# Performance work log

Hardware: AMD Instinct MI355X
Metric: run time of the kernel (lower is better)

## Reference

```python
import jax, jax.numpy as jnp
import numpy as np

B, IN, OUT, P = 512, 4096, 4096, 4
BITS = 4
MAX_INT = float(2 ** (BITS - 1) - 1)  # 7.0


def setup_inputs() -> dict:
    key = jax.random.key(0)
    k1, k2, k3, k4 = jax.random.split(key, 4)
    x = jax.random.normal(k1, (B, IN), dtype=jnp.float32)
    # Cached LFSR-generated pseudo-random matrix, values normalized to [-1, 1]
    U = jax.random.uniform(k2, (OUT * IN, P), dtype=jnp.float32, minval=-1.0, maxval=1.0)
    # 4-bit quantized projection: integers in [-7, 7] stored as float
    q = jnp.round(jnp.clip(jax.random.normal(k3, (P,), dtype=jnp.float32) * 3.0, -MAX_INT, MAX_INT))
    b = jax.random.normal(k4, (OUT,), dtype=jnp.float32)
    return {"x": x, "U": U, "q": q, "b": b, "exponent": 0}


def reference(x, U, q, b, exponent):
    # dequantize: t_hat = q / max_int * 2^exponent  (shared-exponent 4-bit dequant)
    scale = jnp.float32(2.0) ** exponent
    t_hat = q / MAX_INT * scale                      # [P]
    # reconstruct full weight: W = U @ t_hat, reshape to (out, in)
    w = (U @ t_hat).reshape(OUT, IN)                 # [OUT, IN]
    # original layer forward (nn.Linear): y = x @ W^T + b
    return x @ w.T + b                               # [B, OUT]
```

## Files before the change

### kernel.cpp

```cpp
#include <hip/hip_runtime.h>

typedef unsigned short ushort_t;
typedef unsigned int uint_t;
typedef __attribute__((ext_vector_type(4))) float f32x4;
typedef __attribute__((ext_vector_type(8))) short bf16x8;

#define B_DIM 512
#define IN_DIM 4096
#define OUT_DIM 4096
#define BN 32
#define BK 32
#define KSPLIT 4

__device__ __forceinline__ ushort_t f2bf(float f) {
    union { float f; uint_t u; } v; v.f = f;
    uint_t r = v.u + 0x7fffu + ((v.u >> 16) & 1u);
    return (ushort_t)(r >> 16);
}

__global__ __launch_bounds__(256) void conv_x(const float4* __restrict__ X4,
                                              ushort_t* __restrict__ Xb) {
    size_t i = (size_t)blockIdx.x * 256 + threadIdx.x;
    float4 a = X4[i];
    ushort_t r[4] = { f2bf(a.x), f2bf(a.y), f2bf(a.z), f2bf(a.w) };
    *(uint2*)(Xb + i * 4) = *(const uint2*)r;
}

__global__ __launch_bounds__(256, 2) void gemm_pipe(
    const ushort_t* __restrict__ A,
    const float4* __restrict__ U4,
    const float* __restrict__ q,
    const int* __restrict__ expo,
    float* __restrict__ part)
{
    const int M = B_DIM, N = OUT_DIM, K = IN_DIM;
    __shared__ ushort_t sW[2 * BN * BK];

    const int tid  = threadIdx.x;
    const int lane = tid & 63;
    const int wave = tid >> 6;
    const int quad = lane >> 4;
    const int r16  = lane & 15;

    const int n0 = blockIdx.x * BN;
    const int kseg = K / KSPLIT;
    const size_t kbase = (size_t)blockIdx.y * kseg;
    const int nsteps = kseg / BK;

    const float scale = exp2f((float)expo[0]) * (1.0f / 7.0f);
    const float t0 = q[0] * scale, t1 = q[1] * scale,
                t2 = q[2] * scale, t3 = q[3] * scale;

    const float4* gU = U4 + (size_t)(n0 + (tid >> 3)) * K + kbase + (tid & 7) * 4;
    ushort_t* lWb = sW + (tid >> 3) * BK + (tid & 7) * 4;

    const ushort_t* pa = A + (size_t)(wave * 128 + r16) * K + kbase + quad * 8;
    const ushort_t* fb = sW + r16 * BK + quad * 8;

    f32x4 acc[8][2] = {};

    float4 uc[4];
#pragma unroll
    for (int c = 0; c < 4; ++c) uc[c] = gU[c];

#pragma unroll 1
    for (int s = 0; s < nsteps; ++s) {
        bf16x8 av[8];
#pragma unroll
        for (int i = 0; i < 8; ++i)
            av[i] = *(const bf16x8*)(pa + (size_t)i * 16 * K + (size_t)s * BK);

        const size_t koff = (size_t)((s + 1 < nsteps) ? (s + 1) : s) * BK;
        float4 un[4];
#pragma unroll
        for (int c = 0; c < 4; ++c) un[c] = gU[koff + c];

        ushort_t wv[4];
#pragma unroll
        for (int c = 0; c < 4; ++c)
            wv[c] = f2bf(uc[c].x * t0 + uc[c].y * t1 + uc[c].z * t2 + uc[c].w * t3);
        *(uint2*)(lWb + (s & 1) * (BN * BK)) = *(const uint2*)wv;

        asm volatile("s_waitcnt lgkmcnt(0)" ::: "memory");
        __builtin_amdgcn_s_barrier();

        const ushort_t* fbs = fb + (s & 1) * (BN * BK);
        bf16x8 bv0 = *(const bf16x8*)(fbs);
        bf16x8 bv1 = *(const bf16x8*)(fbs + 16 * BK);

#pragma unroll
        for (int i = 0; i < 8; ++i) {
            acc[i][0] = __builtin_amdgcn_mfma_f32_16x16x32_bf16(av[i], bv0, acc[i][0], 0, 0, 0);
            acc[i][1] = __builtin_amdgcn_mfma_f32_16x16x32_bf16(av[i], bv1, acc[i][1], 0, 0, 0);
        }

#pragma unroll
        for (int c = 0; c < 4; ++c) uc[c] = un[c];
    }

    float* outp = part + (size_t)blockIdx.y * M * N;
#pragma unroll
    for (int i = 0; i < 8; ++i) {
        const int mrow = wave * 128 + i * 16 + quad * 4;
#pragma unroll
        for (int j = 0; j < 2; ++j) {
            const int ncol = n0 + j * 16 + r16;
            float* o = outp + (size_t)mrow * N + ncol;
#pragma unroll
            for (int r = 0; r < 4; ++r)
                o[(size_t)r * N] = acc[i][j][r];
        }
    }
}

__global__ __launch_bounds__(256) void reduce_bias(const float4* __restrict__ part,
                                                   const float4* __restrict__ bias,
                                                   float4* __restrict__ out) {
    const int MN4 = (B_DIM * OUT_DIM) / 4;
    int i = blockIdx.x * 256 + threadIdx.x;
    float4 bb = bias[i & 1023];
    float sx = bb.x, sy = bb.y, sz = bb.z, sw = bb.w;
#pragma unroll
    for (int k = 0; k < KSPLIT; ++k) {
        float4 p = part[i + (size_t)k * MN4];
        sx += p.x; sy += p.y; sz += p.z; sw += p.w;
    }
    float4 o; o.x = sx; o.y = sy; o.z = sz; o.w = sw;
    out[i] = o;
}

extern "C" void kernel_launch(void* const* d_in, const int* in_sizes, int n_in,
                              void* d_out, int out_size, void* d_ws, size_t ws_size,
                              hipStream_t stream) {
    const float* x    = (const float*)d_in[0];
    const float* U    = (const float*)d_in[1];
    const float* q    = (const float*)d_in[2];
    const float* b    = (const float*)d_in[3];
    const int*   expo = (const int*)d_in[4];
    float* out = (float*)d_out;

    char* ws = (char*)d_ws;
    ushort_t* Xb  = (ushort_t*)ws;
    float*    prt = (float*)(ws + 4194304);

    conv_x<<<2048, 256, 0, stream>>>((const float4*)x, Xb);
    gemm_pipe<<<dim3(128, KSPLIT), 256, 0, stream>>>(Xb, (const float4*)U,
                                                     q, expo, prt);
    reduce_bias<<<2048, 256, 0, stream>>>((const float4*)prt, (const float4*)b,
                                          (float4*)out);
}
```

Baseline: 419.3 us.

## Widen K stage to 128, use 512-thread blocks, swizzle LDS weight tile

Each stage of the GEMM now covers 128 K-elements instead of 32, so there are 8 stages per split instead of 32 and far fewer barriers. Blocks grow to 8 waves, each handling 64 rows of the batch, and every thread converts 8 float4 U entries per stage. The LDS weight tile uses an XOR swizzle to avoid bank conflicts on the wider rows. The trade-off is more registers per thread for the U prefetch, fewer accumulators per wave, and a different occupancy balance.

```diff
diff --git a/kernel.cpp b/kernel.cpp
--- a/kernel.cpp
+++ b/kernel.cpp
@@ -9,8 +9,9 @@
 #define IN_DIM 4096
 #define OUT_DIM 4096
 #define BN 32
-#define BK 32
+#define BKS 128
 #define KSPLIT 4
+#define NSTAGE 8
 
 __device__ __forceinline__ ushort_t f2bf(float f) {
     union { float f; uint_t u; } v; v.f = f;
@@ -26,7 +27,7 @@
     *(uint2*)(Xb + i * 4) = *(const uint2*)r;
 }
 
-__global__ __launch_bounds__(256, 2) void gemm_pipe(
+__global__ __launch_bounds__(512, 4) void gemm_k(
     const ushort_t* __restrict__ A,
     const float4* __restrict__ U4,
     const float* __restrict__ q,
@@ -34,7 +35,7 @@
     float* __restrict__ part)
 {
     const int M = B_DIM, N = OUT_DIM, K = IN_DIM;
-    __shared__ ushort_t sW[2 * BN * BK];
+    __shared__ ushort_t sW[2 * BN * BKS];
 
     const int tid  = threadIdx.x;
     const int lane = tid & 63;
@@ -45,63 +46,70 @@
     const int n0 = blockIdx.x * BN;
     const int kseg = K / KSPLIT;
     const size_t kbase = (size_t)blockIdx.y * kseg;
-    const int nsteps = kseg / BK;
 
     const float scale = exp2f((float)expo[0]) * (1.0f / 7.0f);
     const float t0 = q[0] * scale, t1 = q[1] * scale,
                 t2 = q[2] * scale, t3 = q[3] * scale;
 
-    const float4* gU = U4 + (size_t)(n0 + (tid >> 3)) * K + kbase + (tid & 7) * 4;
-    ushort_t* lWb = sW + (tid >> 3) * BK + (tid & 7) * 4;
+    const int srow = tid >> 4;
+    const int scol = (tid & 15) * 8;
+    const float4* gU = U4 + (size_t)(n0 + srow) * K + kbase + scol;
+    const int wboff = srow * 256 + ((scol * 2) ^ ((srow & 7) << 4));
 
-    const ushort_t* pa = A + (size_t)(wave * 128 + r16) * K + kbase + quad * 8;
-    const ushort_t* fb = sW + r16 * BK + quad * 8;
+    const ushort_t* pa = A + (size_t)(wave * 64 + r16) * K + kbase + quad * 8;
 
-    f32x4 acc[8][2] = {};
+    const int rswz = (r16 & 7) << 4;
+    const int rb0 = r16 * 256;
+    const int rb1 = (16 + r16) * 256;
 
-    float4 uc[4];
+    f32x4 acc[4][2] = {};
+
+    float4 uc[8];
 #pragma unroll
-    for (int c = 0; c < 4; ++c) uc[c] = gU[c];
+    for (int c = 0; c < 8; ++c) uc[c] = gU[c];
 
 #pragma unroll 1
-    for (int s = 0; s < nsteps; ++s) {
-        bf16x8 av[8];
+    for (int s = 0; s < NSTAGE; ++s) {
+        char* buf = (char*)sW + (s & 1) * (BN * BKS * 2);
+
+        ushort_t wv[8];
 #pragma unroll
-        for (int i = 0; i < 8; ++i)
-            av[i] = *(const bf16x8*)(pa + (size_t)i * 16 * K + (size_t)s * BK);
+        for (int c = 0; c < 8; ++c)
+            wv[c] = f2bf(uc[c].x * t0 + uc[c].y * t1 + uc[c].z * t2 + uc[c].w * t3);
+        *(bf16x8*)(buf + wboff) = *(const bf16x8*)wv;
 
-        const size_t koff = (size_t)((s + 1 < nsteps) ? (s + 1) : s) * BK;
-        float4 un[4];
+        const float4* gUn = (s + 1 < NSTAGE) ? (gU + BKS) : gU;
 #pragma unroll
-        for (int c = 0; c < 4; ++c) un[c] = gU[koff + c];
-
-        ushort_t wv[4];
-#pragma unroll
-        for (int c = 0; c < 4; ++c)
-            wv[c] = f2bf(uc[c].x * t0 + uc[c].y * t1 + uc[c].z * t2 + uc[c].w * t3);
-        *(uint2*)(lWb + (s & 1) * (BN * BK)) = *(const uint2*)wv;
+        for (int c = 0; c < 8; ++c) uc[c] = gUn[c];
+        gU = gUn;
 
         asm volatile("s_waitcnt lgkmcnt(0)" ::: "memory");
         __builtin_amdgcn_s_barrier();
 
-        const ushort_t* fbs = fb + (s & 1) * (BN * BK);
-        bf16x8 bv0 = *(const bf16x8*)(fbs);
-        bf16x8 bv1 = *(const bf16x8*)(fbs + 16 * BK);
+#pragma unroll
+        for (int kk = 0; kk < 4; ++kk) {
+            const int cswz = (kk * 64 + quad * 16) ^ rswz;
+            bf16x8 bv0 = *(const bf16x8*)(buf + rb0 + cswz);
+            bf16x8 bv1 = *(const bf16x8*)(buf + rb1 + cswz);
+
+            bf16x8 av[4];
+            const ushort_t* pak = pa + (size_t)s * BKS + kk * 32;
+#pragma unroll
+            for (int i = 0; i < 4; ++i)
+                av[i] = *(const bf16x8*)(pak + (size_t)i * 16 * K);
 
 #pragma unroll
-        for (int i = 0; i < 8; ++i) {
-            acc[i][0] = __builtin_amdgcn_mfma_f32_16x16x32_bf16(av[i], bv0, acc[i][0], 0, 0, 0);
-            acc[i][1] = __builtin_amdgcn_mfma_f32_16x16x32_bf16(av[i], bv1, acc[i][1], 0, 0, 0);
+            for (int i = 0; i < 4; ++i) {
+                acc[i][0] = __builtin_amdgcn_mfma_f32_16x16x32_bf16(av[i], bv0, acc[i][0], 0, 0, 0);
+                acc[i][1] = __builtin_amdgcn_mfma_f32_16x16x32_bf16(av[i], bv1, acc[i][1], 0, 0, 0);
+            }
         }
-
-#pragma unroll
-        for (int c = 0; c < 4; ++c) uc[c] = un[c];
     }
 
     float* outp = part + (size_t)blockIdx.y * M * N;
 #pragma unroll
-    for (int i = 0; i < 8; ++i) {
-        const int mrow = wave * 128 + i * 16 + quad * 4;
+    for (int i = 0; i < 4; ++i) {
+        const int mrow = wave * 64 + i * 16 + quad * 4;
 #pragma unroll
         for (int j = 0; j < 2; ++j) {
             const int ncol = n0 + j * 16 + r16;
@@ -144,8 +152,8 @@
     float*    prt = (float*)(ws + 4194304);
 
     conv_x<<<2048, 256, 0, stream>>>((const float4*)x, Xb);
-    gemm_pipe<<<dim3(128, KSPLIT), 256, 0, stream>>>(Xb, (const float4*)U,
-                                                     q, expo, prt);
+    gemm_k<<<dim3(128, KSPLIT), 512, 0, stream>>>(Xb, (const float4*)U,
+                                                  q, expo, prt);
     reduce_bias<<<2048, 256, 0, stream>>>((const float4*)prt, (const float4*)b,
                                           (float4*)out);
 }
```

Result: no change. 414.8 us (-1.1%).
